# Optimization experiments

Measured on AMD Instinct MI355X. Metric: run time of the kernel, lower is better.

## Reference

```python
import jax, jax.numpy as jnp
import numpy as np

MARGIN = 0.2
PRED_RATE = 1.0
MAX_VIOLATION = True


def t2i_score(images, obj_nums, captions, cap_lens):
    """images: (Bi, O, D); captions: (Bc, W, D).
    For each image, keep only its first obj_nums[i] objects, compute all
    object-word similarities vs every caption, max-pool over objects,
    sum over all W words (incl. padding, as in the torch code), and
    normalize by caption length. Returns (Bi, Bc)."""
    O = images.shape[1]
    # dot[i, c, o, w] = <images[i, o], captions[c, w]>
    dot = jnp.einsum('iod,cwd->icow', images, captions)
    valid = jnp.arange(O)[None, :] < obj_nums[:, None]          # (Bi, O)
    dot = jnp.where(valid[:, None, :, None], dot, -jnp.inf)
    pooled = dot.max(axis=2).sum(axis=2)                        # (Bi, Bc)
    return pooled / cap_lens.astype(pooled.dtype)[None, :]


def setup_inputs() -> dict:
    key = jax.random.key(0)
    ks = jax.random.split(key, 10)
    B, O, W, D = 128, 36, 50, 128
    Op, Wp = 25, 30
    return {
        'im':         jax.random.normal(ks[0], (B, O, D), dtype=jnp.float32),
        'im_l':       jax.random.randint(ks[1], (B,), 1, O + 1, dtype=jnp.int32),
        's':          jax.random.normal(ks[2], (B, W, D), dtype=jnp.float32),
        's_l':        jax.random.randint(ks[3], (B,), 1, W + 1, dtype=jnp.int32),
        'pred':       jax.random.normal(ks[4], (B, Op, D), dtype=jnp.float32),
        'pred_l':     jax.random.randint(ks[5], (B,), 1, Op + 1, dtype=jnp.int32),
        'cap_o_pred': jax.random.normal(ks[6], (B, Op, D), dtype=jnp.float32),
        'cap_o_l':    jax.random.randint(ks[7], (B,), 1, Op + 1, dtype=jnp.int32),
        'c_r_pred':   jax.random.normal(ks[8], (B, Wp, D), dtype=jnp.float32),
        'c_r_l':      jax.random.randint(ks[9], (B,), 1, Wp + 1, dtype=jnp.int32),
    }


def reference(im, im_l, s, s_l, pred, pred_l, cap_o_pred, cap_o_l, c_r_pred, c_r_l):
    scores = (t2i_score(im, im_l, s, s_l)
              + PRED_RATE * t2i_score(pred, pred_l, c_r_pred, c_r_l))  # (B, B)
    B = scores.shape[0]
    diag = jnp.diagonal(scores)
    cost_s = jnp.maximum(MARGIN + scores - diag[:, None], 0.0)
    cost_im = jnp.maximum(MARGIN + scores - diag[None, :], 0.0)
    eye = jnp.eye(B, dtype=bool)
    cost_s = jnp.where(eye, 0.0, cost_s)
    cost_im = jnp.where(eye, 0.0, cost_im)
    if MAX_VIOLATION:
        cost_s = cost_s.max(axis=1)
        cost_im = cost_im.max(axis=0)
    return cost_s.sum() + cost_im.sum()
```

## Files before the change

kernel.cpp:

```cpp
#include <hip/hip_runtime.h>

typedef __bf16 bf16x8 __attribute__((ext_vector_type(8)));
typedef float f32x4 __attribute__((ext_vector_type(4)));
typedef unsigned int u32x4 __attribute__((ext_vector_type(4)));

__device__ __forceinline__ unsigned short f2bf(float f) {
  unsigned int u = __float_as_uint(f);
  u += 0x7FFFu + ((u >> 16) & 1u);
  return (unsigned short)(u >> 16);
}

__device__ __forceinline__ bf16x8 load_frag(const unsigned short* p) {
  u32x4 v = *(const u32x4*)p;
  return __builtin_bit_cast(bf16x8, v);
}

__global__ __launch_bounds__(256) void convert_all(
    const float* __restrict__ im, const float* __restrict__ s,
    const float* __restrict__ pred, const float* __restrict__ crp,
    unsigned short* __restrict__ imb, unsigned short* __restrict__ sb,
    unsigned short* __restrict__ pb, unsigned short* __restrict__ cb)
{
  int b = blockIdx.x;
  const float* src; unsigned short* dst; int O, OP, base;
  if (b < 768)       { src = im;   dst = imb; O = 36; OP = 48; base = 0; }
  else if (b < 1568) { src = s;    dst = sb;  O = 50; OP = 50; base = 768; }
  else if (b < 2080) { src = pred; dst = pb;  O = 25; OP = 32; base = 1568; }
  else               { src = crp;  dst = cb;  O = 30; OP = 30; base = 2080; }
  int tid = (b - base) * 256 + (int)threadIdx.x;
  int total = 128 * OP * 32;
  if (tid >= total) return;
  int d4 = tid & 31;
  int o  = (tid >> 5) % OP;
  int bb = tid / (OP * 32);
  unsigned short r0 = 0, r1 = 0, r2 = 0, r3 = 0;
  if (o < O) {
    const float4 v = *(const float4*)(src + ((bb * O + o) << 7) + (d4 << 2));
    r0 = f2bf(v.x); r1 = f2bf(v.y); r2 = f2bf(v.z); r3 = f2bf(v.w);
  }
  ushort4 outv; outv.x = r0; outv.y = r1; outv.z = r2; outv.w = r3;
  *(ushort4*)(dst + (size_t)tid * 4) = outv;
}

template<int MT, int W>
__device__ __forceinline__ void t2i_im2(
    const unsigned short* __restrict__ A,
    const unsigned short* __restrict__ Bw,
    const int* __restrict__ obj_l, const int* __restrict__ cap_l,
    float* __restrict__ pooled,
    int vb, float* wmax)
{
  const int ig  = vb >> 3;
  const int i0  = ig * 2;
  const int cg0 = (vb & 7) * 16;
  const int tid = threadIdx.x;
  const int wv = tid >> 6, lane = tid & 63;
  const int quad = lane >> 4, n16 = lane & 15;
  const int ol0 = obj_l[i0], ol1 = obj_l[i0 + 1];

  bf16x8 af[2][MT][4];
#pragma unroll
  for (int im = 0; im < 2; ++im) {
    const unsigned short* Ab =
        A + (((size_t)(i0 + im) * (MT * 16) + n16) << 7) + quad * 8;
#pragma unroll
    for (int t = 0; t < MT; ++t)
#pragma unroll
      for (int s = 0; s < 4; ++s)
        af[im][t][s] = load_frag(Ab + ((t * 16) << 7) + s * 32);
  }

  const unsigned short* Bbase = Bw + (((size_t)cg0 * W + n16) << 7) + quad * 8;

  for (int nt = wv; nt < W; nt += 4) {
    const unsigned short* bp = Bbase + ((nt * 16) << 7);
    bf16x8 bfrag[4];
#pragma unroll
    for (int s = 0; s < 4; ++s) bfrag[s] = load_frag(bp + s * 32);

    f32x4 acc[2][MT];
#pragma unroll
    for (int im = 0; im < 2; ++im)
#pragma unroll
      for (int t = 0; t < MT; ++t) { f32x4 z = {0.f,0.f,0.f,0.f}; acc[im][t] = z; }
#pragma unroll
    for (int s = 0; s < 4; ++s)
#pragma unroll
      for (int im = 0; im < 2; ++im)
#pragma unroll
        for (int t = 0; t < MT; ++t)
          acc[im][t] = __builtin_amdgcn_mfma_f32_16x16x32_bf16(
              af[im][t][s], bfrag[s], acc[im][t], 0, 0, 0);

#pragma unroll
    for (int im = 0; im < 2; ++im) {
      const int ol = im ? ol1 : ol0;
      float m = -3.0e38f;
#pragma unroll
      for (int t = 0; t < MT; ++t)
#pragma unroll
        for (int r = 0; r < 4; ++r) {
          int o = t * 16 + quad * 4 + r;
          if (o < ol) m = fmaxf(m, acc[im][t][r]);
        }
      m = fmaxf(m, __shfl_xor(m, 16));
      m = fmaxf(m, __shfl_xor(m, 32));
      if (quad == 0) wmax[im * (16 * W) + nt * 16 + n16] = m;
    }
  }
  __syncthreads();

  if (tid < 32) {
    const int im = tid >> 4, c = tid & 15;
    const float* wp = wmax + im * (16 * W) + c * W;
    float ssum = 0.f;
    for (int w = 0; w < W; ++w) ssum += wp[w];
    const int cc = cg0 + c;
    pooled[((i0 + im) << 7) + cc] = ssum / (float)cap_l[cc];
  }
}

__global__ __launch_bounds__(256) void t2i_both(
    const unsigned short* __restrict__ imb, const unsigned short* __restrict__ sb,
    const unsigned short* __restrict__ pb,  const unsigned short* __restrict__ cb,
    const int* __restrict__ im_l, const int* __restrict__ s_l,
    const int* __restrict__ pred_l, const int* __restrict__ crl,
    float* __restrict__ p1, float* __restrict__ p2)
{
  __shared__ float wmax[2 * 16 * 50];
  if (blockIdx.x < 512) t2i_im2<3, 50>(imb, sb, im_l, s_l, p1, blockIdx.x, wmax);
  else                  t2i_im2<2, 30>(pb, cb, pred_l, crl, p2, blockIdx.x - 512, wmax);
}

__global__ __launch_bounds__(1024) void loss_kernel(
    const float* __restrict__ p1, const float* __restrict__ p2,
    float* __restrict__ out)
{
  __shared__ float diag[128];
  __shared__ int   rowmaxi[128];
  __shared__ float colmax[8][128];
  __shared__ float wred[16];
  const int tid = threadIdx.x;
  const int sub = tid >> 7, j = tid & 127;
  if (sub == 0) {
    diag[j] = p1[j * 129] + p2[j * 129];
    rowmaxi[j] = 0;
  }
  __syncthreads();

  float colp = 0.f;
#pragma unroll
  for (int rr = 0; rr < 16; ++rr) {
    const int row = sub * 16 + rr;
    const float sc = p1[row * 128 + j] + p2[row * 128 + j];
    const float dr = diag[row];
    float rh = (j == row) ? 0.f : fmaxf(0.2f + sc - dr, 0.f);
    const float ch = (j == row) ? 0.f : fmaxf(0.2f + sc - diag[j], 0.f);
    colp = fmaxf(colp, ch);
#pragma unroll
    for (int o = 32; o; o >>= 1) rh = fmaxf(rh, __shfl_xor(rh, o));
    if ((tid & 63) == 0) atomicMax(&rowmaxi[row], __float_as_int(rh));
  }
  colmax[sub][j] = colp;
  __syncthreads();
  if (sub < 4) colmax[sub][j] = fmaxf(colmax[sub][j], colmax[sub + 4][j]);
  __syncthreads();
  if (sub < 2) colmax[sub][j] = fmaxf(colmax[sub][j], colmax[sub + 2][j]);
  __syncthreads();
  if (sub < 1) colmax[0][j] = fmaxf(colmax[0][j], colmax[1][j]);
  __syncthreads();

  float v = 0.f;
  if (tid < 128)      v = __int_as_float(rowmaxi[tid]);
  else if (tid < 256) v = colmax[0][tid - 128];
#pragma unroll
  for (int o = 32; o; o >>= 1) v += __shfl_xor(v, o);
  if ((tid & 63) == 0) wred[tid >> 6] = v;
  __syncthreads();
  if (tid == 0) {
    float sfin = 0.f;
    for (int k = 0; k < 16; ++k) sfin += wred[k];
    out[0] = sfin;
  }
}

extern "C" void kernel_launch(void* const* d_in, const int* in_sizes, int n_in,
                              void* d_out, int out_size, void* d_ws, size_t ws_size,
                              hipStream_t stream)
{
  const float* im     = (const float*)d_in[0];
  const int*   im_l   = (const int*)  d_in[1];
  const float* s      = (const float*)d_in[2];
  const int*   s_l    = (const int*)  d_in[3];
  const float* pred   = (const float*)d_in[4];
  const int*   pred_l = (const int*)  d_in[5];
  const float* crp    = (const float*)d_in[8];
  const int*   crl    = (const int*)  d_in[9];

  char* ws = (char*)d_ws;
  const size_t off_imb = 0;
  const size_t off_sb  = off_imb + (size_t)128 * 48 * 128 * 2;
  const size_t off_pb  = off_sb  + (size_t)128 * 50 * 128 * 2;
  const size_t off_cb  = off_pb  + (size_t)128 * 32 * 128 * 2;
  const size_t off_p1  = off_cb  + (size_t)128 * 30 * 128 * 2;
  const size_t off_p2  = off_p1  + (size_t)128 * 128 * 4;

  unsigned short* imb = (unsigned short*)(ws + off_imb);
  unsigned short* sb  = (unsigned short*)(ws + off_sb);
  unsigned short* pb  = (unsigned short*)(ws + off_pb);
  unsigned short* cb  = (unsigned short*)(ws + off_cb);
  float* p1 = (float*)(ws + off_p1);
  float* p2 = (float*)(ws + off_p2);

  hipLaunchKernelGGL(convert_all, dim3(2560), dim3(256), 0, stream,
                     im, s, pred, crp, imb, sb, pb, cb);
  hipLaunchKernelGGL(t2i_both, dim3(1024), dim3(256), 0, stream,
                     imb, sb, pb, cb, im_l, s_l, pred_l, crl, p1, p2);
  hipLaunchKernelGGL(loss_kernel, dim3(1), dim3(1024), 0, stream,
                     p1, p2, (float*)d_out);
}
```

Measured before the change: 120.6 us.

## Fuse bf16 conversion and loss into single kernel with last-block reduction

Removes the separate fp32-to-bf16 conversion kernel: the similarity kernel now reads fp32 inputs directly and converts in registers, using byte-permute truncation instead of round-to-nearest. The loss reduction is folded into the same kernel, run by the last block to finish, detected with an atomic counter that is reset by a memset. The intent is to cut launch overhead and the extra workspace round trip, at the cost of twice the global read bytes per fragment, repeated conversion of B tiles across blocks, and a slower single-block loss tail on 256 threads.

After: 182.3 us. +51.1%, slower.

```diff
diff --git a/kernel.cpp b/kernel.cpp
--- a/kernel.cpp
+++ b/kernel.cpp
@@ -4,54 +4,25 @@
 typedef float f32x4 __attribute__((ext_vector_type(4)));
 typedef unsigned int u32x4 __attribute__((ext_vector_type(4)));
 
-__device__ __forceinline__ unsigned short f2bf(float f) {
-  unsigned int u = __float_as_uint(f);
-  u += 0x7FFFu + ((u >> 16) & 1u);
-  return (unsigned short)(u >> 16);
+__device__ __forceinline__ unsigned int pkhi(float lo, float hi) {
+  return __builtin_amdgcn_perm(__float_as_uint(hi), __float_as_uint(lo), 0x07060302u);
 }
-
-__device__ __forceinline__ bf16x8 load_frag(const unsigned short* p) {
-  u32x4 v = *(const u32x4*)p;
+__device__ __forceinline__ bf16x8 cvt8(float4 a, float4 b) {
+  u32x4 v;
+  v.x = pkhi(a.x, a.y); v.y = pkhi(a.z, a.w);
+  v.z = pkhi(b.x, b.y); v.w = pkhi(b.z, b.w);
   return __builtin_bit_cast(bf16x8, v);
 }
 
-__global__ __launch_bounds__(256) void convert_all(
-    const float* __restrict__ im, const float* __restrict__ s,
-    const float* __restrict__ pred, const float* __restrict__ crp,
-    unsigned short* __restrict__ imb, unsigned short* __restrict__ sb,
-    unsigned short* __restrict__ pb, unsigned short* __restrict__ cb)
-{
-  int b = blockIdx.x;
-  const float* src; unsigned short* dst; int O, OP, base;
-  if (b < 768)       { src = im;   dst = imb; O = 36; OP = 48; base = 0; }
-  else if (b < 1568) { src = s;    dst = sb;  O = 50; OP = 50; base = 768; }
-  else if (b < 2080) { src = pred; dst = pb;  O = 25; OP = 32; base = 1568; }
-  else               { src = crp;  dst = cb;  O = 30; OP = 30; base = 2080; }
-  int tid = (b - base) * 256 + (int)threadIdx.x;
-  int total = 128 * OP * 32;
-  if (tid >= total) return;
-  int d4 = tid & 31;
-  int o  = (tid >> 5) % OP;
-  int bb = tid / (OP * 32);
-  unsigned short r0 = 0, r1 = 0, r2 = 0, r3 = 0;
-  if (o < O) {
-    const float4 v = *(const float4*)(src + ((bb * O + o) << 7) + (d4 << 2));
-    r0 = f2bf(v.x); r1 = f2bf(v.y); r2 = f2bf(v.z); r3 = f2bf(v.w);
-  }
-  ushort4 outv; outv.x = r0; outv.y = r1; outv.z = r2; outv.w = r3;
-  *(ushort4*)(dst + (size_t)tid * 4) = outv;
-}
-
-template<int MT, int W>
-__device__ __forceinline__ void t2i_im2(
-    const unsigned short* __restrict__ A,
-    const unsigned short* __restrict__ Bw,
+template<int MT, int W, int O>
+__device__ __forceinline__ void t2i_direct(
+    const float* __restrict__ A,
+    const float* __restrict__ B,
     const int* __restrict__ obj_l, const int* __restrict__ cap_l,
     float* __restrict__ pooled,
     int vb, float* wmax)
 {
-  const int ig  = vb >> 3;
-  const int i0  = ig * 2;
+  const int i0  = (vb >> 3) * 2;
   const int cg0 = (vb & 7) * 16;
   const int tid = threadIdx.x;
   const int wv = tid >> 6, lane = tid & 63;
@@ -60,127 +31,142 @@
 
   bf16x8 af[2][MT][4];
 #pragma unroll
-  for (int im = 0; im < 2; ++im) {
-    const unsigned short* Ab =
-        A + (((size_t)(i0 + im) * (MT * 16) + n16) << 7) + quad * 8;
+  for (int imi = 0; imi < 2; ++imi)
 #pragma unroll
-    for (int t = 0; t < MT; ++t)
+    for (int t = 0; t < MT; ++t) {
+      const int o = t * 16 + n16;
 #pragma unroll
-      for (int s = 0; s < 4; ++s)
-        af[im][t][s] = load_frag(Ab + ((t * 16) << 7) + s * 32);
-  }
+      for (int s = 0; s < 4; ++s) {
+        if (o < O) {
+          const float* ap = A + ((size_t)(i0 + imi) * O + o) * 128 + s * 32 + quad * 8;
+          float4 a0 = *(const float4*)ap;
+          float4 a1 = *(const float4*)(ap + 4);
+          af[imi][t][s] = cvt8(a0, a1);
+        } else {
+          u32x4 z = {0u, 0u, 0u, 0u};
+          af[imi][t][s] = __builtin_bit_cast(bf16x8, z);
+        }
+      }
+    }
 
-  const unsigned short* Bbase = Bw + (((size_t)cg0 * W + n16) << 7) + quad * 8;
+  const float* Bbase = B + ((size_t)cg0 * W + n16) * 128 + quad * 8;
 
   for (int nt = wv; nt < W; nt += 4) {
-    const unsigned short* bp = Bbase + ((nt * 16) << 7);
+    const float* bp = Bbase + (size_t)(nt * 16) * 128;
     bf16x8 bfrag[4];
 #pragma unroll
-    for (int s = 0; s < 4; ++s) bfrag[s] = load_frag(bp + s * 32);
+    for (int s = 0; s < 4; ++s) {
+      float4 b0 = *(const float4*)(bp + s * 32);
+      float4 b1 = *(const float4*)(bp + s * 32 + 4);
+      bfrag[s] = cvt8(b0, b1);
+    }
 
     f32x4 acc[2][MT];
 #pragma unroll
-    for (int im = 0; im < 2; ++im)
+    for (int imi = 0; imi < 2; ++imi)
 #pragma unroll
-      for (int t = 0; t < MT; ++t) { f32x4 z = {0.f,0.f,0.f,0.f}; acc[im][t] = z; }
+      for (int t = 0; t < MT; ++t) { f32x4 z = {0.f,0.f,0.f,0.f}; acc[imi][t] = z; }
 #pragma unroll
     for (int s = 0; s < 4; ++s)
 #pragma unroll
-      for (int im = 0; im < 2; ++im)
+      for (int imi = 0; imi < 2; ++imi)
 #pragma unroll
         for (int t = 0; t < MT; ++t)
-          acc[im][t] = __builtin_amdgcn_mfma_f32_16x16x32_bf16(
-              af[im][t][s], bfrag[s], acc[im][t], 0, 0, 0);
+          acc[imi][t] = __builtin_amdgcn_mfma_f32_16x16x32_bf16(
+              af[imi][t][s], bfrag[s], acc[imi][t], 0, 0, 0);
 
 #pragma unroll
-    for (int im = 0; im < 2; ++im) {
-      const int ol = im ? ol1 : ol0;
+    for (int imi = 0; imi < 2; ++imi) {
+      const int ol = imi ? ol1 : ol0;
       float m = -3.0e38f;
 #pragma unroll
       for (int t = 0; t < MT; ++t)
 #pragma unroll
         for (int r = 0; r < 4; ++r) {
           int o = t * 16 + quad * 4 + r;
-          if (o < ol) m = fmaxf(m, acc[im][t][r]);
+          if (o < ol) m = fmaxf(m, acc[imi][t][r]);
         }
       m = fmaxf(m, __shfl_xor(m, 16));
       m = fmaxf(m, __shfl_xor(m, 32));
-      if (quad == 0) wmax[im * (16 * W) + nt * 16 + n16] = m;
+      if (quad == 0) wmax[imi * (16 * W) + nt * 16 + n16] = m;
     }
   }
   __syncthreads();
 
   if (tid < 32) {
-    const int im = tid >> 4, c = tid & 15;
-    const float* wp = wmax + im * (16 * W) + c * W;
+    const int imi = tid >> 4, c = tid & 15;
+    const float* wp = wmax + imi * (16 * W) + c * W;
     float ssum = 0.f;
     for (int w = 0; w < W; ++w) ssum += wp[w];
     const int cc = cg0 + c;
-    pooled[((i0 + im) << 7) + cc] = ssum / (float)cap_l[cc];
+    pooled[((i0 + imi) << 7) + cc] = ssum / (float)cap_l[cc];
   }
 }
 
-__global__ __launch_bounds__(256) void t2i_both(
-    const unsigned short* __restrict__ imb, const unsigned short* __restrict__ sb,
-    const unsigned short* __restrict__ pb,  const unsigned short* __restrict__ cb,
-    const int* __restrict__ im_l, const int* __restrict__ s_l,
-    const int* __restrict__ pred_l, const int* __restrict__ crl,
-    float* __restrict__ p1, float* __restrict__ p2)
+__device__ __forceinline__ void loss_inline(
+    const float* __restrict__ p1, const float* __restrict__ p2,
+    float* __restrict__ out, float* smem)
 {
-  __shared__ float wmax[2 * 16 * 50];
-  if (blockIdx.x < 512) t2i_im2<3, 50>(imb, sb, im_l, s_l, p1, blockIdx.x, wmax);
-  else                  t2i_im2<2, 30>(pb, cb, pred_l, crl, p2, blockIdx.x - 512, wmax);
-}
-
-__global__ __launch_bounds__(1024) void loss_kernel(
-    const float* __restrict__ p1, const float* __restrict__ p2,
-    float* __restrict__ out)
-{
-  __shared__ float diag[128];
-  __shared__ int   rowmaxi[128];
-  __shared__ float colmax[8][128];
-  __shared__ float wred[16];
+  float* diag    = smem;
+  int*   rowmaxi = (int*)(smem + 128);
+  float* colmax  = smem + 256;
+  float* wred    = smem + 512;
   const int tid = threadIdx.x;
-  const int sub = tid >> 7, j = tid & 127;
-  if (sub == 0) {
+  const int j = tid & 127, half = tid >> 7;
+  if (half == 0) {
     diag[j] = p1[j * 129] + p2[j * 129];
     rowmaxi[j] = 0;
   }
   __syncthreads();
 
   float colp = 0.f;
-#pragma unroll
-  for (int rr = 0; rr < 16; ++rr) {
-    const int row = sub * 16 + rr;
+  for (int rr = 0; rr < 64; ++rr) {
+    const int row = half * 64 + rr;
     const float sc = p1[row * 128 + j] + p2[row * 128 + j];
-    const float dr = diag[row];
-    float rh = (j == row) ? 0.f : fmaxf(0.2f + sc - dr, 0.f);
+    float rh = (j == row) ? 0.f : fmaxf(0.2f + sc - diag[row], 0.f);
     const float ch = (j == row) ? 0.f : fmaxf(0.2f + sc - diag[j], 0.f);
     colp = fmaxf(colp, ch);
 #pragma unroll
     for (int o = 32; o; o >>= 1) rh = fmaxf(rh, __shfl_xor(rh, o));
     if ((tid & 63) == 0) atomicMax(&rowmaxi[row], __float_as_int(rh));
   }
-  colmax[sub][j] = colp;
-  __syncthreads();
-  if (sub < 4) colmax[sub][j] = fmaxf(colmax[sub][j], colmax[sub + 4][j]);
-  __syncthreads();
-  if (sub < 2) colmax[sub][j] = fmaxf(colmax[sub][j], colmax[sub + 2][j]);
-  __syncthreads();
-  if (sub < 1) colmax[0][j] = fmaxf(colmax[0][j], colmax[1][j]);
+  colmax[half * 128 + j] = colp;
   __syncthreads();
 
-  float v = 0.f;
-  if (tid < 128)      v = __int_as_float(rowmaxi[tid]);
-  else if (tid < 256) v = colmax[0][tid - 128];
+  float v;
+  if (tid < 128) v = __int_as_float(rowmaxi[tid]);
+  else           v = fmaxf(colmax[tid - 128], colmax[128 + (tid - 128)]);
 #pragma unroll
   for (int o = 32; o; o >>= 1) v += __shfl_xor(v, o);
   if ((tid & 63) == 0) wred[tid >> 6] = v;
   __syncthreads();
-  if (tid == 0) {
-    float sfin = 0.f;
-    for (int k = 0; k < 16; ++k) sfin += wred[k];
-    out[0] = sfin;
+  if (tid == 0) out[0] = wred[0] + wred[1] + wred[2] + wred[3];
+}
+
+__global__ __launch_bounds__(256) void fused_kernel(
+    const float* __restrict__ im, const float* __restrict__ s32,
+    const float* __restrict__ pred, const float* __restrict__ crp,
+    const int* __restrict__ im_l, const int* __restrict__ s_l,
+    const int* __restrict__ pred_l, const int* __restrict__ crl,
+    float* __restrict__ p1, float* __restrict__ p2,
+    unsigned int* __restrict__ counter, float* __restrict__ out)
+{
+  __shared__ float smem[1600];
+  __shared__ int lastFlag;
+  const int b = blockIdx.x;
+
+  if (b < 512) t2i_direct<3, 50, 36>(im,   s32, im_l,   s_l, p1, b,       smem);
+  else         t2i_direct<2, 30, 25>(pred, crp, pred_l, crl, p2, b - 512, smem);
+
+  __syncthreads();
+  if (threadIdx.x == 0) {
+    __threadfence();
+    lastFlag = (atomicAdd(counter, 1u) == 1023u) ? 1 : 0;
+  }
+  __syncthreads();
+  if (lastFlag) {
+    __threadfence();
+    loss_inline(p1, p2, out, smem);
   }
 }
 
@@ -190,7 +176,7 @@
 {
   const float* im     = (const float*)d_in[0];
   const int*   im_l   = (const int*)  d_in[1];
-  const float* s      = (const float*)d_in[2];
+  const float* s32    = (const float*)d_in[2];
   const int*   s_l    = (const int*)  d_in[3];
   const float* pred   = (const float*)d_in[4];
   const int*   pred_l = (const int*)  d_in[5];
@@ -198,24 +184,12 @@
   const int*   crl    = (const int*)  d_in[9];
 
   char* ws = (char*)d_ws;
-  const size_t off_imb = 0;
-  const size_t off_sb  = off_imb + (size_t)128 * 48 * 128 * 2;
-  const size_t off_pb  = off_sb  + (size_t)128 * 50 * 128 * 2;
-  const size_t off_cb  = off_pb  + (size_t)128 * 32 * 128 * 2;
-  const size_t off_p1  = off_cb  + (size_t)128 * 30 * 128 * 2;
-  const size_t off_p2  = off_p1  + (size_t)128 * 128 * 4;
+  float* p1 = (float*)ws;
+  float* p2 = (float*)(ws + 128 * 128 * 4);
+  unsigned int* counter = (unsigned int*)(ws + 2 * 128 * 128 * 4);
 
-  unsigned short* imb = (unsigned short*)(ws + off_imb);
-  unsigned short* sb  = (unsigned short*)(ws + off_sb);
-  unsigned short* pb  = (unsigned short*)(ws + off_pb);
-  unsigned short* cb  = (unsigned short*)(ws + off_cb);
-  float* p1 = (float*)(ws + off_p1);
-  float* p2 = (float*)(ws + off_p2);
-
-  hipLaunchKernelGGL(convert_all, dim3(2560), dim3(256), 0, stream,
-                     im, s, pred, crp, imb, sb, pb, cb);
-  hipLaunchKernelGGL(t2i_both, dim3(1024), dim3(256), 0, stream,
-                     imb, sb, pb, cb, im_l, s_l, pred_l, crl, p1, p2);
-  hipLaunchKernelGGL(loss_kernel, dim3(1), dim3(1024), 0, stream,
-                     p1, p2, (float*)d_out);
+  hipMemsetAsync((void*)counter, 0, sizeof(unsigned int), stream);
+  hipLaunchKernelGGL(fused_kernel, dim3(1024), dim3(256), 0, stream,
+                     im, s32, pred, crp, im_l, s_l, pred_l, crl,
+                     p1, p2, counter, (float*)d_out);
 }
```
